# Optimization experiments

Measured on AMD Instinct MI355X. Metric: run time of the kernel, lower is better.

## Reference

```python
import jax, jax.numpy as jnp
import numpy as np

N_CTX = 4096
D_MODEL = 2048


def setup_inputs() -> dict:
    key = jax.random.key(0)
    k1, k2, k3 = jax.random.split(key, 3)
    embedding = jax.random.normal(k1, (N_CTX, D_MODEL), dtype=jnp.float32)
    # torch.rand -> uniform [0, 1)
    qk = jax.random.uniform(k2, (D_MODEL, D_MODEL), dtype=jnp.float32)
    ov = jax.random.uniform(k3, (D_MODEL, D_MODEL), dtype=jnp.float32)
    return {"embedding": embedding, "qk": qk, "ov": ov}


def reference(embedding, qk, ov):
    n = embedding.shape[0]
    # scores[i, j] = e_i @ qk @ e_j  -> [N, N]
    scores = (embedding @ qk) @ embedding.T
    # strict upper triangle gets -inf (causal mask), matching triu(-inf, diag=1)
    causal_mask = jnp.triu(jnp.full((n, n), -jnp.inf, dtype=scores.dtype), k=1)
    scores = scores + causal_mask
    attn = jax.nn.softmax(scores, axis=-1)  # nn.Softmax() on 2D -> dim=1
    return (attn @ embedding) @ ov
```

## Files before the change

### kernel.cpp

```cpp
#include <hip/hip_runtime.h>
#include <hip/hip_bf16.h>
#include <math.h>

#define N_CTX 4096
#define DM    2048

typedef __attribute__((ext_vector_type(8))) short short8;
typedef __attribute__((ext_vector_type(4))) float f32x4;
typedef unsigned short ushort_t;

__device__ __forceinline__ ushort_t f2bf(float x) {
    __hip_bfloat16 h = __float2bfloat16(x);
    return __builtin_bit_cast(ushort_t, h);
}
__device__ __forceinline__ float bf2f(ushort_t u) {
    return __bfloat162float(__builtin_bit_cast(__hip_bfloat16, u));
}

__device__ __forceinline__ void gload16(const void* g, void* l) {
    __builtin_amdgcn_global_load_lds((const __attribute__((address_space(1))) void*)g,
                                     (__attribute__((address_space(3))) void*)l,
                                     16, 0, 0);
}


__global__ __launch_bounds__(256) void split_cast_kernel(
    const float* __restrict__ in, ushort_t* __restrict__ hi, ushort_t* __restrict__ lo, int n4)
{
    int idx = blockIdx.x * 256 + threadIdx.x;
    if (idx >= n4) return;
    float4 v = reinterpret_cast<const float4*>(in)[idx];
    float vv[4] = {v.x, v.y, v.z, v.w};
    ushort_t h[4], l[4];
#pragma unroll
    for (int j = 0; j < 4; ++j) {
        h[j] = f2bf(vv[j]);
        l[j] = f2bf(vv[j] - bf2f(h[j]));
    }
    reinterpret_cast<ushort4*>(hi)[idx] = *reinterpret_cast<ushort4*>(h);
    reinterpret_cast<ushort4*>(lo)[idx] = *reinterpret_cast<ushort4*>(l);
}

template <bool SPLIT>
__global__ __launch_bounds__(256) void transpose_cast_kernel(
    const float* __restrict__ in, ushort_t* __restrict__ hi, ushort_t* __restrict__ lo,
    int R, int C)
{
    __shared__ float tile[32][33];
    int bc = blockIdx.x * 32;
    int br = blockIdx.y * 32;
    int tx = threadIdx.x, ty = threadIdx.y;
#pragma unroll
    for (int r = ty; r < 32; r += 8)
        tile[r][tx] = in[(size_t)(br + r) * C + bc + tx];
    __syncthreads();
#pragma unroll
    for (int c = ty; c < 32; c += 8) {
        float v = tile[tx][c];
        size_t o = (size_t)(bc + c) * R + br + tx;
        ushort_t h = f2bf(v);
        hi[o] = h;
        if (SPLIT) lo[o] = f2bf(v - bf2f(h));
    }
}


template <int OM, bool TRI>
__global__ __launch_bounds__(256, 2) void gemm_split_kernel(
    const ushort_t* __restrict__ Ah, const ushort_t* __restrict__ Al,
    const ushort_t* __restrict__ Bh, const ushort_t* __restrict__ Bl,
    int K, int ldc,
    float* __restrict__ Cf, ushort_t* __restrict__ Ch, ushort_t* __restrict__ Cl)
{
    int bx, by;
    if (TRI) {
        int i = blockIdx.x;
        int b = (int)((sqrtf(8.f * (float)i + 1.f) - 1.f) * 0.5f);
        while ((b + 1) * (b + 2) / 2 <= i) ++b;
        while (b * (b + 1) / 2 > i) --b;
        by = b; bx = i - b * (b + 1) / 2;
    } else {
        bx = blockIdx.x; by = blockIdx.y;
    }

    __shared__ ushort_t lds[2][4][128 * 32];

    const int t = threadIdx.x;
    const int l = t & 63;
    const int w = t >> 6;
    const int wr = w >> 1;
    const int wc = w & 1;
    const int lr = l & 15;
    const int lc = l >> 4;

    f32x4 acc[4][4];
#pragma unroll
    for (int m = 0; m < 4; ++m)
#pragma unroll
        for (int n = 0; n < 4; ++n) acc[m][n] = (f32x4){0.f, 0.f, 0.f, 0.f};

    const size_t arow0 = (size_t)by * 128;
    const size_t brow0 = (size_t)bx * 128;

    auto stg1 = [&](const ushort_t* src, ushort_t* dst, size_t row0, int kt) {
#pragma unroll
        for (int i2 = 0; i2 < 2; ++i2) {
            int f = i2 * 256 + t;
            int r = f >> 2, c = f & 3;
            gload16(src + (row0 + r) * (size_t)K + kt + ((c ^ ((r >> 1) & 3)) << 3),
                    (char*)dst + f * 16);
        }
    };
    auto stage = [&](int kt, int buf) {
        stg1(Ah, lds[buf][0], arow0, kt);
        stg1(Al, lds[buf][1], arow0, kt);
        stg1(Bh, lds[buf][2], brow0, kt);
        stg1(Bl, lds[buf][3], brow0, kt);
    };
    auto rdf = [&](short8* d, const ushort_t* base, int rbase) {
#pragma unroll
        for (int m = 0; m < 4; ++m) {
            int row = rbase + m * 16 + lr;
            d[m] = *(const short8*)((const char*)base + row * 64 +
                                    ((lc ^ ((row >> 1) & 3)) << 4));
        }
    };
    auto mm16 = [&](const short8* a, const short8* b) {
#pragma unroll
        for (int m = 0; m < 4; ++m)
#pragma unroll
            for (int n = 0; n < 4; ++n)
                acc[m][n] = __builtin_amdgcn_mfma_f32_16x16x32_bf16(
                    a[m], b[n], acc[m][n], 0, 0, 0);
    };

    stage(0, 0);
    __syncthreads();
    const int nt = K >> 5;
    for (int tt = 0; tt < nt; ++tt) {
        const int buf = tt & 1;
        if (tt + 1 < nt) stage((tt + 1) << 5, buf ^ 1);
        short8 ah[4], bh[4], x[4];
        rdf(ah, lds[buf][0], wr * 64);
        rdf(bh, lds[buf][2], wc * 64);
        mm16(ah, bh);
        rdf(x, lds[buf][3], wc * 64);
        mm16(ah, x);
        rdf(x, lds[buf][1], wr * 64);
        mm16(x, bh);
        __syncthreads();
    }

    const int r0 = by * 128 + wr * 64 + (lc << 2);
    const int c0 = bx * 128 + wc * 64 + lr;
#pragma unroll
    for (int m = 0; m < 4; ++m)
#pragma unroll
        for (int n = 0; n < 4; ++n)
#pragma unroll
            for (int j = 0; j < 4; ++j) {
                size_t o = (size_t)(r0 + m * 16 + j) * ldc + (c0 + n * 16);
                float v = acc[m][n][j];
                if (OM == 0) {
                    Cf[o] = v;
                } else {
                    ushort_t hh = f2bf(v);
                    Ch[o] = hh;
                    Cl[o] = f2bf(v - bf2f(hh));
                }
            }
}


template <int OM, bool CKLIM>
__global__ __launch_bounds__(256, 2) void gemm_bt_kernel(
    const ushort_t* __restrict__ A, const ushort_t* __restrict__ B,
    int K, int ldc,
    float* __restrict__ Cf, ushort_t* __restrict__ Ch)
{
    const int bx = blockIdx.x;
    const int by = blockIdx.y;

    __shared__ ushort_t lds[2][2][128 * 64];

    const int t = threadIdx.x;
    const int l = t & 63;
    const int w = t >> 6;
    const int wr = w >> 1;
    const int wc = w & 1;

    f32x4 acc[4][4];
#pragma unroll
    for (int m = 0; m < 4; ++m)
#pragma unroll
        for (int n = 0; n < 4; ++n) acc[m][n] = (f32x4){0.f, 0.f, 0.f, 0.f};

    const size_t arow0 = (size_t)by * 128;
    const size_t brow0 = (size_t)bx * 128;

    int kend = K;
    if (CKLIM) { int lim = (by + 1) * 128; if (lim < kend) kend = lim; }

    auto stage = [&](int kt, int buf) {
#pragma unroll
        for (int i2 = 0; i2 < 4; ++i2) {
            int f = i2 * 256 + t;
            int r = f >> 3, c = f & 7;
            gload16(A + (arow0 + r) * (size_t)K + kt + ((c ^ (r & 7)) << 3),
                    (char*)lds[buf][0] + f * 16);
            gload16(B + (brow0 + r) * (size_t)K + kt + ((c ^ (r & 7)) << 3),
                    (char*)lds[buf][1] + f * 16);
        }
    };

    stage(0, 0);
    __syncthreads();
    const int nt = kend >> 6;
    for (int tt = 0; tt < nt; ++tt) {
        const int buf = tt & 1;
        if (tt + 1 < nt) stage((tt + 1) << 6, buf ^ 1);
#pragma unroll
        for (int kk = 0; kk < 2; ++kk) {
            short8 af[4], bfr[4];
#pragma unroll
            for (int m = 0; m < 4; ++m) {
                int row = wr * 64 + m * 16 + (l & 15);
                int gby = kk * 64 + (l >> 4) * 16;
                af[m] = *(const short8*)((const char*)lds[buf][0] + row * 128 +
                                         (gby ^ ((row & 7) * 16)));
            }
#pragma unroll
            for (int n = 0; n < 4; ++n) {
                int row = wc * 64 + n * 16 + (l & 15);
                int gby = kk * 64 + (l >> 4) * 16;
                bfr[n] = *(const short8*)((const char*)lds[buf][1] + row * 128 +
                                          (gby ^ ((row & 7) * 16)));
            }
#pragma unroll
            for (int m = 0; m < 4; ++m)
#pragma unroll
                for (int n = 0; n < 4; ++n)
                    acc[m][n] = __builtin_amdgcn_mfma_f32_16x16x32_bf16(
                        af[m], bfr[n], acc[m][n], 0, 0, 0);
        }
        __syncthreads();
    }

    const int r0 = by * 128 + wr * 64 + ((l >> 4) << 2);
    const int c0 = bx * 128 + wc * 64 + (l & 15);
#pragma unroll
    for (int m = 0; m < 4; ++m)
#pragma unroll
        for (int n = 0; n < 4; ++n)
#pragma unroll
            for (int j = 0; j < 4; ++j) {
                size_t o = (size_t)(r0 + m * 16 + j) * ldc + (c0 + n * 16);
                if (OM == 0) Cf[o] = acc[m][n][j];
                else         Ch[o] = f2bf(acc[m][n][j]);
            }
}


__device__ __forceinline__ float waveMax(float v) {
#pragma unroll
    for (int o = 32; o > 0; o >>= 1) v = fmaxf(v, __shfl_xor(v, o, 64));
    return v;
}
__device__ __forceinline__ float waveSum(float v) {
#pragma unroll
    for (int o = 32; o > 0; o >>= 1) v += __shfl_xor(v, o, 64);
    return v;
}

__global__ __launch_bounds__(256) void softmax_kernel(
    const float* __restrict__ S, ushort_t* __restrict__ A)
{
    const int i = blockIdx.x;
    __shared__ float row[N_CTX];
    __shared__ float red[8];
    const int t = threadIdx.x;
    const int len = i + 1;
    const float* Srow = S + (size_t)i * N_CTX;

    float m = -3.4e38f;
    for (int j = t; j < len; j += 256) {
        float v = Srow[j];
        row[j] = v;
        m = fmaxf(m, v);
    }
    m = waveMax(m);
    if ((t & 63) == 0) red[t >> 6] = m;
    __syncthreads();
    m = fmaxf(fmaxf(red[0], red[1]), fmaxf(red[2], red[3]));

    float s = 0.f;
    for (int j = t; j < len; j += 256) {
        float e = __expf(row[j] - m);
        row[j] = e;
        s += e;
    }
    s = waveSum(s);
    __syncthreads();
    if ((t & 63) == 0) red[t >> 6] = s;
    __syncthreads();
    float inv = 1.f / (red[0] + red[1] + red[2] + red[3]);

    ushort_t* Arow = A + (size_t)i * N_CTX;
    for (int j = t; j < N_CTX; j += 256)
        Arow[j] = (j < len) ? f2bf(row[j] * inv) : (ushort_t)0;
}


extern "C" void kernel_launch(void* const* d_in, const int* in_sizes, int n_in,
                              void* d_out, int out_size, void* d_ws, size_t ws_size,
                              hipStream_t stream)
{
    const float* E  = (const float*)d_in[0];
    const float* qk = (const float*)d_in[1];
    const float* ov = (const float*)d_in[2];
    float* out = (float*)d_out;

    char* ws = (char*)d_ws;
    size_t off = 0;
    auto take = [&](size_t bytes) -> char* {
        char* p = ws + off;
        off += (bytes + 255) & ~(size_t)255;
        return p;
    };

    ushort_t* Ehi   = (ushort_t*)take((size_t)N_CTX * DM * 2);
    ushort_t* Elo   = (ushort_t*)take((size_t)N_CTX * DM * 2);
    ushort_t* Et    = (ushort_t*)take((size_t)N_CTX * DM * 2);
    ushort_t* QKthi = (ushort_t*)take((size_t)DM * DM * 2);
    ushort_t* QKtlo = (ushort_t*)take((size_t)DM * DM * 2);
    ushort_t* OVt   = (ushort_t*)take((size_t)DM * DM * 2);
    ushort_t* Qhi   = (ushort_t*)take((size_t)N_CTX * DM * 2);
    ushort_t* Qlo   = (ushort_t*)take((size_t)N_CTX * DM * 2);
    float*    S     = (float*)take((size_t)N_CTX * N_CTX * 4);
    ushort_t* Attn  = (ushort_t*)take((size_t)N_CTX * N_CTX * 2);
    ushort_t* Hbf   = (ushort_t*)take((size_t)N_CTX * DM * 2);
    (void)ws_size; (void)in_sizes; (void)n_in; (void)out_size;

    split_cast_kernel<<<dim3((N_CTX * DM / 4) / 256), 256, 0, stream>>>(E, Ehi, Elo, N_CTX * DM / 4);
    transpose_cast_kernel<true ><<<dim3(DM / 32, DM / 32),    dim3(32, 8), 0, stream>>>(qk, QKthi, QKtlo, DM, DM);
    transpose_cast_kernel<false><<<dim3(DM / 32, DM / 32),    dim3(32, 8), 0, stream>>>(ov, OVt, nullptr, DM, DM);
    transpose_cast_kernel<false><<<dim3(DM / 32, N_CTX / 32), dim3(32, 8), 0, stream>>>(E, Et, nullptr, N_CTX, DM);

    gemm_split_kernel<2, false><<<dim3(DM / 128, N_CTX / 128), 256, 0, stream>>>(
        Ehi, Elo, QKthi, QKtlo, DM, DM, nullptr, Qhi, Qlo);

    gemm_split_kernel<0, true><<<dim3(32 * 33 / 2), 256, 0, stream>>>(
        Qhi, Qlo, Ehi, Elo, DM, N_CTX, S, nullptr, nullptr);

    softmax_kernel<<<N_CTX, 256, 0, stream>>>(S, Attn);

    gemm_bt_kernel<1, true><<<dim3(DM / 128, N_CTX / 128), 256, 0, stream>>>(
        Attn, Et, N_CTX, DM, nullptr, Hbf);

    gemm_bt_kernel<0, false><<<dim3(DM / 128, N_CTX / 128), 256, 0, stream>>>(
        Hbf, OVt, DM, DM, out, nullptr);
}
```

Baseline: 460.1 us.

## Enlarge split-bf16 GEMM tiles to 256x128 with 512 threads and dynamic LDS

The split-precision GEMM now uses 256x128 output tiles computed by 8 waves (512 threads), with the A hi/lo tiles shared across twice as many rows of output. LDS becomes dynamic (96 KB, double-buffered). The causal scores GEMM switches from a packed triangular block index to a 2D grid with early exit for fully masked tiles. The aim is more reuse of the B tile per load and fewer blocks. In exchange, the larger LDS footprint and wave count may cut occupancy, and coarser causal tiles compute more masked work.

```diff
diff --git a/kernel.cpp b/kernel.cpp
--- a/kernel.cpp
+++ b/kernel.cpp
@@ -65,25 +65,18 @@
 }
 
 
-template <int OM, bool TRI>
-__global__ __launch_bounds__(256, 2) void gemm_split_kernel(
+template <int OM, bool CAUSAL>
+__global__ __launch_bounds__(512, 2) void gemm_split_kernel(
     const ushort_t* __restrict__ Ah, const ushort_t* __restrict__ Al,
     const ushort_t* __restrict__ Bh, const ushort_t* __restrict__ Bl,
     int K, int ldc,
     float* __restrict__ Cf, ushort_t* __restrict__ Ch, ushort_t* __restrict__ Cl)
 {
-    int bx, by;
-    if (TRI) {
-        int i = blockIdx.x;
-        int b = (int)((sqrtf(8.f * (float)i + 1.f) - 1.f) * 0.5f);
-        while ((b + 1) * (b + 2) / 2 <= i) ++b;
-        while (b * (b + 1) / 2 > i) --b;
-        by = b; bx = i - b * (b + 1) / 2;
-    } else {
-        bx = blockIdx.x; by = blockIdx.y;
-    }
-
-    __shared__ ushort_t lds[2][4][128 * 32];
+    const int bx = blockIdx.x;
+    const int by = blockIdx.y;
+    if (CAUSAL && bx * 128 > by * 256 + 255) return;
+
+    extern __shared__ char lds[];
 
     const int t = threadIdx.x;
     const int l = t & 63;
@@ -99,30 +92,35 @@
 #pragma unroll
         for (int n = 0; n < 4; ++n) acc[m][n] = (f32x4){0.f, 0.f, 0.f, 0.f};
 
-    const size_t arow0 = (size_t)by * 128;
+    const size_t arow0 = (size_t)by * 256;
     const size_t brow0 = (size_t)bx * 128;
 
-    auto stg1 = [&](const ushort_t* src, ushort_t* dst, size_t row0, int kt) {
+    auto stgA = [&](const ushort_t* src, char* dst, int kt) {
 #pragma unroll
         for (int i2 = 0; i2 < 2; ++i2) {
-            int f = i2 * 256 + t;
+            int f = i2 * 512 + t;
             int r = f >> 2, c = f & 3;
-            gload16(src + (row0 + r) * (size_t)K + kt + ((c ^ ((r >> 1) & 3)) << 3),
-                    (char*)dst + f * 16);
+            gload16(src + (arow0 + r) * (size_t)K + kt + ((c ^ ((r >> 1) & 3)) << 3),
+                    dst + f * 16);
         }
     };
+    auto stgB = [&](const ushort_t* src, char* dst, int kt) {
+        int r = t >> 2, c = t & 3;
+        gload16(src + (brow0 + r) * (size_t)K + kt + ((c ^ ((r >> 1) & 3)) << 3),
+                dst + t * 16);
+    };
     auto stage = [&](int kt, int buf) {
-        stg1(Ah, lds[buf][0], arow0, kt);
-        stg1(Al, lds[buf][1], arow0, kt);
-        stg1(Bh, lds[buf][2], brow0, kt);
-        stg1(Bl, lds[buf][3], brow0, kt);
-    };
-    auto rdf = [&](short8* d, const ushort_t* base, int rbase) {
+        char* base = lds + buf * 49152;
+        stgA(Ah, base, kt);
+        stgA(Al, base + 16384, kt);
+        stgB(Bh, base + 32768, kt);
+        stgB(Bl, base + 40960, kt);
+    };
+    auto rdf = [&](short8* d, const char* base, int rbase) {
 #pragma unroll
         for (int m = 0; m < 4; ++m) {
             int row = rbase + m * 16 + lr;
-            d[m] = *(const short8*)((const char*)base + row * 64 +
-                                    ((lc ^ ((row >> 1) & 3)) << 4));
+            d[m] = *(const short8*)(base + row * 64 + ((lc ^ ((row >> 1) & 3)) << 4));
         }
     };
     auto mm16 = [&](const short8* a, const short8* b) {
@@ -139,19 +137,20 @@
     const int nt = K >> 5;
     for (int tt = 0; tt < nt; ++tt) {
         const int buf = tt & 1;
+        const char* base = lds + buf * 49152;
         if (tt + 1 < nt) stage((tt + 1) << 5, buf ^ 1);
         short8 ah[4], bh[4], x[4];
-        rdf(ah, lds[buf][0], wr * 64);
-        rdf(bh, lds[buf][2], wc * 64);
+        rdf(ah, base, wr * 64);
+        rdf(bh, base + 32768, wc * 64);
         mm16(ah, bh);
-        rdf(x, lds[buf][3], wc * 64);
+        rdf(x, base + 40960, wc * 64);
         mm16(ah, x);
-        rdf(x, lds[buf][1], wr * 64);
+        rdf(x, base + 16384, wr * 64);
         mm16(x, bh);
         __syncthreads();
     }
 
-    const int r0 = by * 128 + wr * 64 + (lc << 2);
+    const int r0 = by * 256 + wr * 64 + (lc << 2);
     const int c0 = bx * 128 + wc * 64 + lr;
 #pragma unroll
     for (int m = 0; m < 4; ++m)
@@ -341,15 +340,21 @@
     ushort_t* Hbf   = (ushort_t*)take((size_t)N_CTX * DM * 2);
     (void)ws_size; (void)in_sizes; (void)n_in; (void)out_size;
 
+    constexpr int SMEM = 96 * 1024;
+    hipFuncSetAttribute((const void*)&gemm_split_kernel<2, false>,
+                        hipFuncAttributeMaxDynamicSharedMemorySize, SMEM);
+    hipFuncSetAttribute((const void*)&gemm_split_kernel<0, true>,
+                        hipFuncAttributeMaxDynamicSharedMemorySize, SMEM);
+
     split_cast_kernel<<<dim3((N_CTX * DM / 4) / 256), 256, 0, stream>>>(E, Ehi, Elo, N_CTX * DM / 4);
     transpose_cast_kernel<true ><<<dim3(DM / 32, DM / 32),    dim3(32, 8), 0, stream>>>(qk, QKthi, QKtlo, DM, DM);
     transpose_cast_kernel<false><<<dim3(DM / 32, DM / 32),    dim3(32, 8), 0, stream>>>(ov, OVt, nullptr, DM, DM);
     transpose_cast_kernel<false><<<dim3(DM / 32, N_CTX / 32), dim3(32, 8), 0, stream>>>(E, Et, nullptr, N_CTX, DM);
 
-    gemm_split_kernel<2, false><<<dim3(DM / 128, N_CTX / 128), 256, 0, stream>>>(
+    gemm_split_kernel<2, false><<<dim3(DM / 128, N_CTX / 256), 512, SMEM, stream>>>(
         Ehi, Elo, QKthi, QKtlo, DM, DM, nullptr, Qhi, Qlo);
 
-    gemm_split_kernel<0, true><<<dim3(32 * 33 / 2), 256, 0, stream>>>(
+    gemm_split_kernel<0, true><<<dim3(N_CTX / 128, N_CTX / 256), 512, SMEM, stream>>>(
         Qhi, Qlo, Ehi, Elo, DM, N_CTX, S, nullptr, nullptr);
 
     softmax_kernel<<<N_CTX, 256, 0, stream>>>(S, Attn);
```

After: 475.6 us. +3.4%, slower.
